# Kernel tuning notes

Hardware: AMD Instinct MI355X
Metric: run time of the kernel (lower is better)

## Reference

```python
import jax, jax.numpy as jnp
import numpy as np
from jax.ops import segment_sum, segment_max

N_NODES = 100000
N_EDGES = 3200000
NODE_FEAT = 128
EDGE_DIM = 8
H = 4          # heads for all three layers
C_HID = 8      # out_layer_1 == out_layer_2 == 8
N_CLASSES = 1
NEG_SLOPE = 0.2


def setup_inputs() -> dict:
    key = jax.random.key(0)
    ks = jax.random.split(key, 20)
    g = lambda k, shape, fan: jax.random.normal(k, shape, jnp.float32) / np.sqrt(fan)
    inp = {
        "x": jax.random.normal(ks[0], (N_NODES, NODE_FEAT), jnp.float32),
        "edge_attr": jax.random.normal(ks[1], (N_EDGES, EDGE_DIM), jnp.float32),
        "edge_index": jax.random.randint(ks[2], (2, N_EDGES), 0, N_NODES, jnp.int32),
        # layer 1: node_feat -> H*C_HID, concat=True, with edge features
        "W1": g(ks[3], (NODE_FEAT, H * C_HID), NODE_FEAT),
        "a_src1": g(ks[4], (H, C_HID), C_HID),
        "a_dst1": g(ks[5], (H, C_HID), C_HID),
        "We1": g(ks[6], (EDGE_DIM, H * C_HID), EDGE_DIM),
        "a_e1": g(ks[7], (H, C_HID), C_HID),
        "b1": jnp.zeros((H * C_HID,), jnp.float32),
        # layer 2: H*C_HID -> C_HID, concat=False
        "W2": g(ks[8], (H * C_HID, H * C_HID), H * C_HID),
        "a_src2": g(ks[9], (H, C_HID), C_HID),
        "a_dst2": g(ks[10], (H, C_HID), C_HID),
        "b2": jnp.zeros((C_HID,), jnp.float32),
        # layer 3: C_HID -> N_CLASSES, concat=False
        "W3": g(ks[11], (C_HID, H * N_CLASSES), C_HID),
        "a_src3": g(ks[12], (H, N_CLASSES), 1),
        "a_dst3": g(ks[13], (H, N_CLASSES), 1),
        "b3": jnp.zeros((N_CLASSES,), jnp.float32),
    }
    return inp


def _gat_conv(x, src, dst, W, a_src, a_dst, bias, concat,
              edge_attr=None, W_edge=None, a_edge=None):
    """PyG GATConv forward (eval mode). src/dst already include self-loops."""
    n = x.shape[0]
    h, c = a_src.shape
    xh = (x @ W).reshape(n, h, c)                       # [N,H,C]
    alpha = (xh * a_src[None]).sum(-1)[src] \
          + (xh * a_dst[None]).sum(-1)[dst]             # [E,H]
    if edge_attr is not None:
        eh = (edge_attr @ W_edge).reshape(-1, h, c)     # [E,H,C]
        alpha = alpha + (eh * a_edge[None]).sum(-1)
    alpha = jax.nn.leaky_relu(alpha, NEG_SLOPE)
    # segment softmax over incoming edges of each dst node
    amax = segment_max(alpha, dst, num_segments=n)       # [N,H]
    ex = jnp.exp(alpha - amax[dst])
    denom = segment_sum(ex, dst, num_segments=n)
    alpha = ex / (denom[dst] + 1e-16)                    # [E,H]
    out = segment_sum(alpha[:, :, None] * xh[src], dst, num_segments=n)  # [N,H,C]
    out = out.reshape(n, h * c) if concat else out.mean(axis=1)
    return out + bias


def _add_self_loops(edge_index, n):
    loop = jnp.arange(n, dtype=edge_index.dtype)
    src = jnp.concatenate([edge_index[0], loop])
    dst = jnp.concatenate([edge_index[1], loop])
    return src, dst


def reference(x, edge_attr, edge_index, W1, a_src1, a_dst1, We1, a_e1, b1,
              W2, a_src2, a_dst2, b2, W3, a_src3, a_dst3, b3):
    n = x.shape[0]
    src, dst = _add_self_loops(edge_index, n)
    # self-loop edge_attr: fill_value='mean' => scatter-mean of edge_attr by dst
    deg = segment_sum(jnp.ones((edge_index.shape[1],), x.dtype), edge_index[1],
                      num_segments=n)
    mean_attr = segment_sum(edge_attr, edge_index[1], num_segments=n) \
              / jnp.maximum(deg, 1.0)[:, None]
    ea = jnp.concatenate([edge_attr, mean_attr], axis=0)

    h = _gat_conv(x, src, dst, W1, a_src1, a_dst1, b1, True,
                  edge_attr=ea, W_edge=We1, a_edge=a_e1)
    h = jax.nn.elu(h)
    h = _gat_conv(h, src, dst, W2, a_src2, a_dst2, b2, False)
    h = jax.nn.elu(h)
    out = _gat_conv(h, src, dst, W3, a_src3, a_dst3, b3, False)
    return out
```

## Files before the change

kernel.cpp:

```cpp
#include <hip/hip_runtime.h>
#include <hip/hip_fp16.h>
#include <cmath>

static inline int cdiv(long a, int b){ return (int)((a + b - 1) / b); }

__device__ __forceinline__ float lrelu(float x){ return x > 0.f ? x : 0.2f * x; }
__device__ __forceinline__ float elu1(float x){ return x > 0.f ? x : expm1f(x); }
__device__ __forceinline__ float fexp(float x){ return __expf(x); }
__device__ __forceinline__ float sel4(float4 v, int h){
  float ab = (h & 1) ? v.y : v.x;
  float cd = (h & 1) ? v.w : v.z;
  return (h & 2) ? cd : ab;
}

#define WAVE_FENCE() do { asm volatile("" ::: "memory"); __builtin_amdgcn_sched_barrier(0); } while(0)

#define W_SHIFT 7
#define BUCKET_N (1 << W_SHIFT)
#define NBMAX   1024
#define NCHUNKS 1024
#define CH_MAX  3136
#define MS_THREADS 1024



__global__ __launch_bounds__(MS_THREADS)
void hist_chunks_kernel(const int* __restrict__ ei, int E, int CH, int* __restrict__ hist2d){
  __shared__ int s_b[NBMAX];
  int t = threadIdx.x, chunk = blockIdx.x;
  s_b[t] = 0;
  __syncthreads();
  int lo = chunk * CH, hi = min(lo + CH, E);
  for (int e = lo + t; e < hi; e += MS_THREADS)
    atomicAdd(&s_b[ei[E + e] >> W_SHIFT], 1);
  __syncthreads();
  hist2d[(size_t)chunk * NBMAX + t] = s_b[t];
}

__global__ __launch_bounds__(NCHUNKS)
void col_scan_kernel(int* __restrict__ hist2d, int* __restrict__ bcnt){
  __shared__ int s[NCHUNKS];
  int b = blockIdx.x, t = threadIdx.x;
  int v = hist2d[(size_t)t * NBMAX + b];
  s[t] = v; __syncthreads();
  #pragma unroll
  for (int off = 1; off < NCHUNKS; off <<= 1){
    int u = (t >= off) ? s[t - off] : 0;
    __syncthreads();
    s[t] += u;
    __syncthreads();
  }
  hist2d[(size_t)t * NBMAX + b] = s[t] - v;
  if (t == NCHUNKS - 1) bcnt[b] = s[t];
}

__global__ void scan_buckets_kernel(const int* __restrict__ bcnt, int nb, int total,
                                    int* __restrict__ bstart, int* __restrict__ row_start, int n){
  __shared__ int s[1024];
  int t = threadIdx.x;
  int v = (t < nb) ? bcnt[t] : 0;
  s[t] = v; __syncthreads();
  #pragma unroll
  for (int off = 1; off < 1024; off <<= 1){
    int u = (t >= off) ? s[t - off] : 0;
    __syncthreads();
    s[t] += u;
    __syncthreads();
  }
  bstart[t] = (t < nb) ? s[t] - v : total;
  if (t == 0){ bstart[NBMAX] = total; row_start[n] = total; }
}

__global__ void wevec_kernel(const float* __restrict__ We, const float* __restrict__ ae,
                             float* __restrict__ wev){
  int i = threadIdx.x;
  if (i >= 32) return;
  int d = i >> 2, h = i & 3;
  float acc = 0.f;
  #pragma unroll
  for (int c = 0; c < 8; ++c) acc = fmaf(We[d * 32 + h * 8 + c], ae[h * 8 + c], acc);
  wev[d * 4 + h] = acc;
}

__global__ __launch_bounds__(MS_THREADS)
void multisplit_kernel(const int* __restrict__ ei, int E, int CH,
                       const float* __restrict__ eattr, const float* __restrict__ wev,
                       const int* __restrict__ bstart, const int* __restrict__ prefix2d,
                       int4* __restrict__ staged){
  __shared__ int4 s_rec[CH_MAX];
  __shared__ int s_fill[NBMAX];
  __shared__ int s_lbase[NBMAX];
  __shared__ int s_shift[NBMAX];
  __shared__ float s_wev[32];
  int t = threadIdx.x, chunk = blockIdx.x;
  if (t < 32) s_wev[t] = wev[t];
  s_fill[t] = 0;
  __syncthreads();
  int lo = chunk * CH, hi = min(lo + CH, E);
  int cnt = hi - lo;
  for (int e = lo + t; e < hi; e += MS_THREADS)
    atomicAdd(&s_fill[ei[E + e] >> W_SHIFT], 1);
  __syncthreads();
  int v = s_fill[t];
  s_lbase[t] = v; __syncthreads();
  #pragma unroll
  for (int off = 1; off < NBMAX; off <<= 1){
    int u = (t >= off) ? s_lbase[t - off] : 0;
    __syncthreads();
    s_lbase[t] += u;
    __syncthreads();
  }
  int excl = s_lbase[t] - v;
  s_lbase[t] = excl;
  s_shift[t] = bstart[t] + prefix2d[(size_t)chunk * NBMAX + t] - excl;
  s_fill[t] = 0;
  __syncthreads();
  for (int e = lo + t; e < hi; e += MS_THREADS){
    int d = ei[E + e];
    int b = d >> W_SHIFT;
    const float4* ea = (const float4*)(eattr + (size_t)e * 8);
    float4 v0 = ea[0], v1 = ea[1];
    float av[8] = {v0.x, v0.y, v0.z, v0.w, v1.x, v1.y, v1.z, v1.w};
    float e0 = 0, e1 = 0, e2 = 0, e3 = 0;
    #pragma unroll
    for (int k = 0; k < 8; ++k){
      e0 = fmaf(av[k], s_wev[k * 4 + 0], e0);
      e1 = fmaf(av[k], s_wev[k * 4 + 1], e1);
      e2 = fmaf(av[k], s_wev[k * 4 + 2], e2);
      e3 = fmaf(av[k], s_wev[k * 4 + 3], e3);
    }
    __half2 h01 = __floats2half2_rn(e0, e1);
    __half2 h23 = __floats2half2_rn(e2, e3);
    int pos = s_lbase[b] + atomicAdd(&s_fill[b], 1);
    s_rec[pos] = make_int4(ei[e], d,
                           __builtin_bit_cast(int, h01), __builtin_bit_cast(int, h23));
  }
  __syncthreads();
  for (int i = t; i < cnt; i += MS_THREADS){
    int4 r = s_rec[i];
    staged[s_shift[r.y >> W_SHIFT] + i] = r;
  }
}

__global__ __launch_bounds__(MS_THREADS)
void bucket_scatter_kernel(const int* __restrict__ bstart, const int4* __restrict__ staged,
                           int n, int* __restrict__ row_start, int* __restrict__ srcs,
                           uint2* __restrict__ escp, float4* __restrict__ selfesc){
  __shared__ int s_cnt[BUCKET_N];
  __shared__ int s_cur[BUCKET_N];
  __shared__ int s_start[BUCKET_N];
  int b = blockIdx.x, t = threadIdx.x;
  int node0 = b << W_SHIFT;
  if (t < BUCKET_N) s_cnt[t] = 0;
  __syncthreads();
  int lo = bstart[b], hi = bstart[b + 1];
  for (int i = lo + t; i < hi; i += MS_THREADS)
    atomicAdd(&s_cnt[staged[i].y & (BUCKET_N - 1)], 1);
  __syncthreads();
  if (t < BUCKET_N) s_cur[t] = s_cnt[t];
  __syncthreads();
  #pragma unroll
  for (int off = 1; off < BUCKET_N; off <<= 1){
    int v = (t < BUCKET_N && t >= off) ? s_cur[t - off] : 0;
    __syncthreads();
    if (t < BUCKET_N) s_cur[t] += v;
    __syncthreads();
  }
  if (t < BUCKET_N){
    int excl = s_cur[t] - s_cnt[t];
    int nd = node0 + t;
    if (nd <= n) row_start[nd] = lo + excl;
    s_start[t] = lo + excl;
    s_cur[t] = lo + excl;
  }
  __syncthreads();
  for (int i = lo + t; i < hi; i += MS_THREADS){
    int4 r = staged[i];
    int pos = atomicAdd(&s_cur[r.y & (BUCKET_N - 1)], 1);
    srcs[pos] = r.x;
    escp[pos] = make_uint2((unsigned)r.z, (unsigned)r.w);
  }
  __syncthreads();
  int nl = t >> 3, sub = t & 7;
  int nd2 = node0 + nl;
  if (nd2 >= n) return;
  int r0 = s_start[nl], r1 = s_start[nl] + s_cnt[nl];
  float e0 = 0, e1 = 0, e2 = 0, e3 = 0;
  for (int k = r0 + sub; k < r1; k += 8){
    uint2 u = escp[k];
    float2 f01 = __half22float2(__builtin_bit_cast(__half2, u.x));
    float2 f23 = __half22float2(__builtin_bit_cast(__half2, u.y));
    e0 += f01.x; e1 += f01.y; e2 += f23.x; e3 += f23.y;
  }
  #pragma unroll
  for (int off = 1; off < 8; off <<= 1){
    e0 += __shfl_xor(e0, off, 64); e1 += __shfl_xor(e1, off, 64);
    e2 += __shfl_xor(e2, off, 64); e3 += __shfl_xor(e3, off, 64);
  }
  if (sub == 0){
    float inv = 1.f / fmaxf((float)s_cnt[nl], 1.f);
    selfesc[nd2] = make_float4(e0 * inv, e1 * inv, e2 * inv, e3 * inv);
  }
}

template<int K>
__global__ __launch_bounds__(256)
void gemm_score_tiled(const float* __restrict__ A, const float* __restrict__ W,
                      const float* __restrict__ asrc, const float* __restrict__ adst,
                      float* __restrict__ out, float* __restrict__ sS,
                      float* __restrict__ sD, int n){
  constexpr int KH = (K > 64) ? 64 : K;
  constexpr int K4 = KH / 4;
  __shared__ float s_AT[KH * 128];
  __shared__ float s_W[K * 32];
  __shared__ float s_as[32], s_ad[32];
  int t = threadIdx.x;
  for (int i = t; i < K * 32; i += 256) s_W[i] = W[i];
  if (t < 32){ s_as[t] = asrc[t]; s_ad[t] = adst[t]; }
  int n0 = blockIdx.x * 128;
  int nrows = min(128, n - n0);
  int rg = t >> 3, q = t & 7;
  float4 acc[4] = {{0,0,0,0},{0,0,0,0},{0,0,0,0},{0,0,0,0}};

  for (int k0 = 0; k0 < K; k0 += KH){
    __syncthreads();
    #pragma unroll
    for (int it = 0; it < 128 * K4 / 256; ++it){
      int idx = t + it * 256;
      int row = idx & 127, k4 = idx >> 7;
      if (row < nrows){
        float4 v = *(const float4*)(A + (size_t)(n0 + row) * K + k0 + 4 * k4);
        s_AT[(4 * k4 + 0) * 128 + row] = v.x;
        s_AT[(4 * k4 + 1) * 128 + row] = v.y;
        s_AT[(4 * k4 + 2) * 128 + row] = v.z;
        s_AT[(4 * k4 + 3) * 128 + row] = v.w;
      }
    }
    __syncthreads();
    #pragma unroll 4
    for (int k = 0; k < KH; ++k){
      float4 a4 = *(const float4*)(s_AT + k * 128 + 4 * rg);
      float4 w4 = *(const float4*)(s_W + (k0 + k) * 32 + 4 * q);
      acc[0].x = fmaf(a4.x, w4.x, acc[0].x); acc[0].y = fmaf(a4.x, w4.y, acc[0].y);
      acc[0].z = fmaf(a4.x, w4.z, acc[0].z); acc[0].w = fmaf(a4.x, w4.w, acc[0].w);
      acc[1].x = fmaf(a4.y, w4.x, acc[1].x); acc[1].y = fmaf(a4.y, w4.y, acc[1].y);
      acc[1].z = fmaf(a4.y, w4.z, acc[1].z); acc[1].w = fmaf(a4.y, w4.w, acc[1].w);
      acc[2].x = fmaf(a4.z, w4.x, acc[2].x); acc[2].y = fmaf(a4.z, w4.y, acc[2].y);
      acc[2].z = fmaf(a4.z, w4.z, acc[2].z); acc[2].w = fmaf(a4.z, w4.w, acc[2].w);
      acc[3].x = fmaf(a4.w, w4.x, acc[3].x); acc[3].y = fmaf(a4.w, w4.y, acc[3].y);
      acc[3].z = fmaf(a4.w, w4.z, acc[3].z); acc[3].w = fmaf(a4.w, w4.w, acc[3].w);
    }
  }

  float as0 = s_as[4 * q + 0], as1 = s_as[4 * q + 1], as2 = s_as[4 * q + 2], as3 = s_as[4 * q + 3];
  float ad0 = s_ad[4 * q + 0], ad1 = s_ad[4 * q + 1], ad2 = s_ad[4 * q + 2], ad3 = s_ad[4 * q + 3];
  #pragma unroll
  for (int i = 0; i < 4; ++i){
    int row = n0 + 4 * rg + i;
    bool ok = (4 * rg + i) < nrows;
    if (ok) ((float4*)out)[(size_t)row * 8 + q] = acc[i];
    float ps = acc[i].x * as0 + acc[i].y * as1 + acc[i].z * as2 + acc[i].w * as3;
    float pd = acc[i].x * ad0 + acc[i].y * ad1 + acc[i].z * ad2 + acc[i].w * ad3;
    ps += __shfl_xor(ps, 1, 64);
    pd += __shfl_xor(pd, 1, 64);
    if (ok && !(q & 1)){
      sS[(size_t)row * 4 + (q >> 1)] = ps;
      sD[(size_t)row * 4 + (q >> 1)] = pd;
    }
  }
}

template<int MODE, bool EDGE>
__global__ void gather_kernel(const int* __restrict__ row_start, const int* __restrict__ srcs,
                              const uint2* __restrict__ escp, const float4* __restrict__ selfesc,
                              const float* __restrict__ sS, const float* __restrict__ sD,
                              const float* __restrict__ xh, const float* __restrict__ bias,
                              float* __restrict__ out, int n,
                              const float* __restrict__ W3p, const float* __restrict__ as3p,
                              const float* __restrict__ ad3p, float* __restrict__ xh3,
                              float* __restrict__ ss3, float* __restrict__ sd3){
  int wv = threadIdx.x >> 6, lane = threadIdx.x & 63;
  int node = blockIdx.x * 4 + wv;

  if constexpr (MODE == 2){
    if (node >= n) return;
    int rs = row_start[node], deg = row_start[node + 1] - rs;
    float4 sd4 = ((const float4*)sD)[node];
    float4 acc = {0,0,0,0}, dsum = {0,0,0,0};
    for (int k = lane; k < deg; k += 64){
      int s = srcs[rs + k];
      float4 ss = ((const float4*)sS)[s];
      float4 w;
      w.x = fexp(lrelu(ss.x + sd4.x)); w.y = fexp(lrelu(ss.y + sd4.y));
      w.z = fexp(lrelu(ss.z + sd4.z)); w.w = fexp(lrelu(ss.w + sd4.w));
      dsum.x += w.x; dsum.y += w.y; dsum.z += w.z; dsum.w += w.w;
      float4 xv = ((const float4*)xh)[s];
      acc.x = fmaf(w.x, xv.x, acc.x); acc.y = fmaf(w.y, xv.y, acc.y);
      acc.z = fmaf(w.z, xv.z, acc.z); acc.w = fmaf(w.w, xv.w, acc.w);
    }
    #pragma unroll
    for (int off = 1; off < 64; off <<= 1){
      acc.x += __shfl_xor(acc.x, off, 64); acc.y += __shfl_xor(acc.y, off, 64);
      acc.z += __shfl_xor(acc.z, off, 64); acc.w += __shfl_xor(acc.w, off, 64);
      dsum.x += __shfl_xor(dsum.x, off, 64); dsum.y += __shfl_xor(dsum.y, off, 64);
      dsum.z += __shfl_xor(dsum.z, off, 64); dsum.w += __shfl_xor(dsum.w, off, 64);
    }
    if (lane == 0){
      float4 ssn = ((const float4*)sS)[node];
      float4 wsf;
      wsf.x = fexp(lrelu(ssn.x + sd4.x)); wsf.y = fexp(lrelu(ssn.y + sd4.y));
      wsf.z = fexp(lrelu(ssn.z + sd4.z)); wsf.w = fexp(lrelu(ssn.w + sd4.w));
      float4 xvn = ((const float4*)xh)[node];
      float v = (acc.x + wsf.x * xvn.x) / (dsum.x + wsf.x + 1e-16f)
              + (acc.y + wsf.y * xvn.y) / (dsum.y + wsf.y + 1e-16f)
              + (acc.z + wsf.z * xvn.z) / (dsum.z + wsf.z + 1e-16f)
              + (acc.w + wsf.w * xvn.w) / (dsum.w + wsf.w + 1e-16f);
      out[node] = 0.25f * v + bias[0];
    }
    return;
  } else {
  __shared__ float4 s_w[4][64];
  __shared__ int    s_src[4][64];
  __shared__ float  s_w3[32];
  __shared__ float  s_a3[8];
  if constexpr (MODE == 1){
    if (threadIdx.x < 32) s_w3[threadIdx.x] = W3p[threadIdx.x];
    if (threadIdx.x < 8)
      s_a3[threadIdx.x] = (threadIdx.x < 4) ? as3p[threadIdx.x] : ad3p[threadIdx.x - 4];
    __syncthreads();
  }
  if (node >= n) return;
  int rs = row_start[node], deg = row_start[node + 1] - rs;
  float4 sd4 = ((const float4*)sD)[node];
  int q = lane & 7;
  int h = q >> 1;
  int sg = lane >> 3;
  float4 acc = {0,0,0,0};
  float dacc = 0.f;

  for (int base = 0; base < deg; base += 64){
    int k = base + lane;
    float4 w = {0,0,0,0}; int s = 0;
    if (k < deg){
      s = srcs[rs + k];
      float4 ss = ((const float4*)sS)[s];
      float a0 = ss.x + sd4.x, a1 = ss.y + sd4.y, a2 = ss.z + sd4.z, a3 = ss.w + sd4.w;
      if constexpr (EDGE){
        uint2 u = escp[rs + k];
        float2 f01 = __half22float2(__builtin_bit_cast(__half2, u.x));
        float2 f23 = __half22float2(__builtin_bit_cast(__half2, u.y));
        a0 += f01.x; a1 += f01.y; a2 += f23.x; a3 += f23.y;
      }
      w.x = fexp(lrelu(a0)); w.y = fexp(lrelu(a1));
      w.z = fexp(lrelu(a2)); w.w = fexp(lrelu(a3));
    }
    s_w[wv][lane] = w;
    s_src[wv][lane] = s;
    WAVE_FENCE();
    int nvalid = min(deg - base, 64);
    const float* s_wf = (const float*)&s_w[wv][0];
    #pragma unroll
    for (int i = 0; i < 8; ++i){
      int slot = i * 8 + sg;
      if (slot < nvalid){
        int s2 = s_src[wv][slot];
        float wg = s_wf[slot * 4 + h];
        float4 xv = ((const float4*)xh)[(size_t)s2 * 8 + q];
        dacc += wg;
        acc.x = fmaf(wg, xv.x, acc.x); acc.y = fmaf(wg, xv.y, acc.y);
        acc.z = fmaf(wg, xv.z, acc.z); acc.w = fmaf(wg, xv.w, acc.w);
      }
    }
    WAVE_FENCE();
  }

  #pragma unroll
  for (int off = 8; off < 64; off <<= 1){
    acc.x += __shfl_xor(acc.x, off, 64); acc.y += __shfl_xor(acc.y, off, 64);
    acc.z += __shfl_xor(acc.z, off, 64); acc.w += __shfl_xor(acc.w, off, 64);
    dacc  += __shfl_xor(dacc,  off, 64);
  }
  float4 ssn = ((const float4*)sS)[node];
  float a_self = sel4(ssn, h) + sel4(sd4, h);
  if constexpr (EDGE) a_self += sel4(selfesc[node], h);
  float wsel = fexp(lrelu(a_self));
  float4 xvn = ((const float4*)xh)[(size_t)node * 8 + q];
  acc.x = fmaf(wsel, xvn.x, acc.x); acc.y = fmaf(wsel, xvn.y, acc.y);
  acc.z = fmaf(wsel, xvn.z, acc.z); acc.w = fmaf(wsel, xvn.w, acc.w);
  dacc += wsel;
  float rin = 1.f / (dacc + 1e-16f);
  float4 val = {acc.x * rin, acc.y * rin, acc.z * rin, acc.w * rin};

  if constexpr (MODE == 0){
    float4 b4 = ((const float4*)bias)[q];
    val.x = elu1(val.x + b4.x); val.y = elu1(val.y + b4.y);
    val.z = elu1(val.z + b4.z); val.w = elu1(val.w + b4.w);
    if (lane < 8) ((float4*)out)[(size_t)node * 8 + lane] = val;
  } else {
    val.x += __shfl_xor(val.x, 2, 64); val.y += __shfl_xor(val.y, 2, 64);
    val.z += __shfl_xor(val.z, 2, 64); val.w += __shfl_xor(val.w, 2, 64);
    val.x += __shfl_xor(val.x, 4, 64); val.y += __shfl_xor(val.y, 4, 64);
    val.z += __shfl_xor(val.z, 4, 64); val.w += __shfl_xor(val.w, 4, 64);
    float4 b4 = ((const float4*)bias)[q & 1];
    val.x = elu1(val.x * 0.25f + b4.x); val.y = elu1(val.y * 0.25f + b4.y);
    val.z = elu1(val.z * 0.25f + b4.z); val.w = elu1(val.w * 0.25f + b4.w);
    float4 oth;
    oth.x = __shfl_xor(val.x, 1, 64); oth.y = __shfl_xor(val.y, 1, 64);
    oth.z = __shfl_xor(val.z, 1, 64); oth.w = __shfl_xor(val.w, 1, 64);
    float h2v[8];
    if (q & 1){
      h2v[0] = oth.x; h2v[1] = oth.y; h2v[2] = oth.z; h2v[3] = oth.w;
      h2v[4] = val.x; h2v[5] = val.y; h2v[6] = val.z; h2v[7] = val.w;
    } else {
      h2v[0] = val.x; h2v[1] = val.y; h2v[2] = val.z; h2v[3] = val.w;
      h2v[4] = oth.x; h2v[5] = oth.y; h2v[6] = oth.z; h2v[7] = oth.w;
    }
    float x3[4];
    #pragma unroll
    for (int j = 0; j < 4; ++j){
      float a = 0.f;
      #pragma unroll
      for (int k = 0; k < 8; ++k) a = fmaf(h2v[k], s_w3[k * 4 + j], a);
      x3[j] = a;
    }
    if (lane == 0){
      ((float4*)xh3)[node] = make_float4(x3[0], x3[1], x3[2], x3[3]);
      ((float4*)ss3)[node] = make_float4(x3[0] * s_a3[0], x3[1] * s_a3[1],
                                         x3[2] * s_a3[2], x3[3] * s_a3[3]);
      ((float4*)sd3)[node] = make_float4(x3[0] * s_a3[4], x3[1] * s_a3[5],
                                         x3[2] * s_a3[6], x3[3] * s_a3[7]);
    }
  }
  }
}


extern "C" void kernel_launch(void* const* d_in, const int* in_sizes, int n_in,
                              void* d_out, int out_size, void* d_ws, size_t ws_size,
                              hipStream_t stream){
  const float* x     = (const float*)d_in[0];
  const float* eattr = (const float*)d_in[1];
  const int*   ei    = (const int*)d_in[2];
  const float* W1  = (const float*)d_in[3];
  const float* as1 = (const float*)d_in[4];
  const float* ad1 = (const float*)d_in[5];
  const float* We1 = (const float*)d_in[6];
  const float* ae1 = (const float*)d_in[7];
  const float* b1  = (const float*)d_in[8];
  const float* W2  = (const float*)d_in[9];
  const float* as2 = (const float*)d_in[10];
  const float* ad2 = (const float*)d_in[11];
  const float* b2  = (const float*)d_in[12];
  const float* W3  = (const float*)d_in[13];
  const float* as3 = (const float*)d_in[14];
  const float* ad3 = (const float*)d_in[15];
  const float* b3  = (const float*)d_in[16];

  const int N = in_sizes[0] / 128;
  const int E = in_sizes[2] / 2;
  const int nb_buckets = (N + BUCKET_N - 1) >> W_SHIFT;
  const int CH = cdiv(E, NCHUNKS);

  char* b0 = (char*)d_ws;
  int4* staged = (int4*)b0;
  float* fp = (float*)b0;
  float* xh = fp; fp += (size_t)N * 32;
  float* sS = fp; fp += (size_t)N * 4;
  float* sD = fp; fp += (size_t)N * 4;
  float* h1 = fp; fp += (size_t)N * 32;
  int*  srcs = (int*)(b0 + (size_t)E * 16);
  uint2* escp = (uint2*)(b0 + (size_t)E * 20);
  int* hist2d = (int*)(b0 + (size_t)E * 28);
  float4* selfesc = (float4*)(hist2d + (size_t)NCHUNKS * NBMAX);
  float* xh3 = (float*)(selfesc + N);
  float* ss3 = xh3 + (size_t)N * 4;
  float* sd3 = ss3 + (size_t)N * 4;
  int* ip = (int*)(sd3 + (size_t)N * 4);
  int* bcnt      = ip; ip += NBMAX;
  int* bstart    = ip; ip += NBMAX + 1;
  int* row_start = ip; ip += N + 1;
  float* wev = (float*)ip;

  const int B = 256;

  wevec_kernel<<<1, 32, 0, stream>>>(We1, ae1, wev);
  hist_chunks_kernel<<<NCHUNKS, MS_THREADS, 0, stream>>>(ei, E, CH, hist2d);
  col_scan_kernel<<<nb_buckets, NCHUNKS, 0, stream>>>(hist2d, bcnt);
  scan_buckets_kernel<<<1, 1024, 0, stream>>>(bcnt, nb_buckets, E, bstart, row_start, N);
  multisplit_kernel<<<NCHUNKS, MS_THREADS, 0, stream>>>(ei, E, CH, eattr, wev, bstart, hist2d, staged);
  bucket_scatter_kernel<<<nb_buckets, MS_THREADS, 0, stream>>>(bstart, staged, N, row_start, srcs, escp, selfesc);

  gemm_score_tiled<128><<<cdiv(N, 128), B, 0, stream>>>(x, W1, as1, ad1, xh, sS, sD, N);
  gather_kernel<0,true><<<cdiv(N, 4), B, 0, stream>>>(row_start, srcs, escp, selfesc, sS, sD, xh, b1, h1, N,
                                                      nullptr, nullptr, nullptr, nullptr, nullptr, nullptr);

  gemm_score_tiled<32><<<cdiv(N, 128), B, 0, stream>>>(h1, W2, as2, ad2, xh, sS, sD, N);
  gather_kernel<1,false><<<cdiv(N, 4), B, 0, stream>>>(row_start, srcs, escp, selfesc, sS, sD, xh, b2, nullptr, N,
                                                       W3, as3, ad3, xh3, ss3, sd3);

  gather_kernel<2,false><<<cdiv(N, 4), B, 0, stream>>>(row_start, srcs, escp, selfesc, ss3, sd3, xh3, b3, (float*)d_out, N,
                                                       nullptr, nullptr, nullptr, nullptr, nullptr, nullptr);
}
```

Baseline: 385.8 us.

## Recompute attention scores in gather from features, drop precomputed score arrays

Removes the precomputed per-node source/destination score arrays. Each gather lane now recomputes the attention logit from the gathered neighbour feature row, using a shuffle to combine half-heads. The attention vectors and edge weights are pre-scaled by log2(e) so exp2 replaces exp, and leaky ReLU becomes a max. The two-phase shared-memory weight staging in the gather is replaced by a direct per-group loop over 8 edges at a time. This cuts one random gather per edge and some GEMM epilogue writes, but adds a few FMAs and a shuffle per edge, plus a cross-lane dependency in the inner loop.

```diff
diff --git a/kernel.cpp b/kernel.cpp
--- a/kernel.cpp
+++ b/kernel.cpp
@@ -4,16 +4,14 @@
 
 static inline int cdiv(long a, int b){ return (int)((a + b - 1) / b); }
 
-__device__ __forceinline__ float lrelu(float x){ return x > 0.f ? x : 0.2f * x; }
+__device__ __forceinline__ float lrelu(float x){ return fmaxf(x, 0.2f * x); }
 __device__ __forceinline__ float elu1(float x){ return x > 0.f ? x : expm1f(x); }
-__device__ __forceinline__ float fexp(float x){ return __expf(x); }
+__device__ __forceinline__ float fexp2(float x){ return exp2f(x); }
 __device__ __forceinline__ float sel4(float4 v, int h){
   float ab = (h & 1) ? v.y : v.x;
   float cd = (h & 1) ? v.w : v.z;
   return (h & 2) ? cd : ab;
 }
-
-#define WAVE_FENCE() do { asm volatile("" ::: "memory"); __builtin_amdgcn_sched_barrier(0); } while(0)
 
 #define W_SHIFT 7
 #define BUCKET_N (1 << W_SHIFT)
@@ -71,15 +69,28 @@
   if (t == 0){ bstart[NBMAX] = total; row_start[n] = total; }
 }
 
-__global__ void wevec_kernel(const float* __restrict__ We, const float* __restrict__ ae,
-                             float* __restrict__ wev){
+__global__ void prep_kernel(const float* __restrict__ We, const float* __restrict__ ae,
+                            const float* __restrict__ as1, const float* __restrict__ ad1,
+                            const float* __restrict__ as2, const float* __restrict__ ad2,
+                            const float* __restrict__ as3, const float* __restrict__ ad3,
+                            float* __restrict__ wev, float* __restrict__ avecs){
+  const float L2E = 1.4426950408889634f;
   int i = threadIdx.x;
-  if (i >= 32) return;
-  int d = i >> 2, h = i & 3;
-  float acc = 0.f;
-  #pragma unroll
-  for (int c = 0; c < 8; ++c) acc = fmaf(We[d * 32 + h * 8 + c], ae[h * 8 + c], acc);
-  wev[d * 4 + h] = acc;
+  if (i < 32){
+    int d = i >> 2, h = i & 3;
+    float acc = 0.f;
+    #pragma unroll
+    for (int c = 0; c < 8; ++c) acc = fmaf(We[d * 32 + h * 8 + c], ae[h * 8 + c], acc);
+    wev[d * 4 + h] = acc * L2E;
+    avecs[i]      = as1[i] * L2E;
+    avecs[32 + i] = ad1[i] * L2E;
+    avecs[64 + i] = as2[i] * L2E;
+    avecs[96 + i] = ad2[i] * L2E;
+  }
+  if (i < 4){
+    avecs[128 + i] = as3[i] * L2E;
+    avecs[132 + i] = ad3[i] * L2E;
+  }
 }
 
 __global__ __launch_bounds__(MS_THREADS)
@@ -205,18 +216,14 @@
 
 template<int K>
 __global__ __launch_bounds__(256)
-void gemm_score_tiled(const float* __restrict__ A, const float* __restrict__ W,
-                      const float* __restrict__ asrc, const float* __restrict__ adst,
-                      float* __restrict__ out, float* __restrict__ sS,
-                      float* __restrict__ sD, int n){
+void gemm_tiled(const float* __restrict__ A, const float* __restrict__ W,
+                float* __restrict__ out, int n){
   constexpr int KH = (K > 64) ? 64 : K;
   constexpr int K4 = KH / 4;
   __shared__ float s_AT[KH * 128];
   __shared__ float s_W[K * 32];
-  __shared__ float s_as[32], s_ad[32];
   int t = threadIdx.x;
   for (int i = t; i < K * 32; i += 256) s_W[i] = W[i];
-  if (t < 32){ s_as[t] = asrc[t]; s_ad[t] = adst[t]; }
   int n0 = blockIdx.x * 128;
   int nrows = min(128, n - n0);
   int rg = t >> 3, q = t & 7;
@@ -251,50 +258,39 @@
       acc[3].z = fmaf(a4.w, w4.z, acc[3].z); acc[3].w = fmaf(a4.w, w4.w, acc[3].w);
     }
   }
-
-  float as0 = s_as[4 * q + 0], as1 = s_as[4 * q + 1], as2 = s_as[4 * q + 2], as3 = s_as[4 * q + 3];
-  float ad0 = s_ad[4 * q + 0], ad1 = s_ad[4 * q + 1], ad2 = s_ad[4 * q + 2], ad3 = s_ad[4 * q + 3];
   #pragma unroll
   for (int i = 0; i < 4; ++i){
     int row = n0 + 4 * rg + i;
-    bool ok = (4 * rg + i) < nrows;
-    if (ok) ((float4*)out)[(size_t)row * 8 + q] = acc[i];
-    float ps = acc[i].x * as0 + acc[i].y * as1 + acc[i].z * as2 + acc[i].w * as3;
-    float pd = acc[i].x * ad0 + acc[i].y * ad1 + acc[i].z * ad2 + acc[i].w * ad3;
-    ps += __shfl_xor(ps, 1, 64);
-    pd += __shfl_xor(pd, 1, 64);
-    if (ok && !(q & 1)){
-      sS[(size_t)row * 4 + (q >> 1)] = ps;
-      sD[(size_t)row * 4 + (q >> 1)] = pd;
-    }
+    if ((4 * rg + i) < nrows) ((float4*)out)[(size_t)row * 8 + q] = acc[i];
   }
 }
 
 template<int MODE, bool EDGE>
 __global__ void gather_kernel(const int* __restrict__ row_start, const int* __restrict__ srcs,
                               const uint2* __restrict__ escp, const float4* __restrict__ selfesc,
-                              const float* __restrict__ sS, const float* __restrict__ sD,
-                              const float* __restrict__ xh, const float* __restrict__ bias,
-                              float* __restrict__ out, int n,
-                              const float* __restrict__ W3p, const float* __restrict__ as3p,
-                              const float* __restrict__ ad3p, float* __restrict__ xh3,
-                              float* __restrict__ ss3, float* __restrict__ sd3){
+                              const float* __restrict__ xh, const float* __restrict__ avq,
+                              const float* __restrict__ bias, float* __restrict__ out, int n,
+                              const float* __restrict__ W3p, float* __restrict__ xh3){
   int wv = threadIdx.x >> 6, lane = threadIdx.x & 63;
   int node = blockIdx.x * 4 + wv;
 
   if constexpr (MODE == 2){
     if (node >= n) return;
     int rs = row_start[node], deg = row_start[node + 1] - rs;
-    float4 sd4 = ((const float4*)sD)[node];
+    float4 a3s = *(const float4*)avq;
+    float4 a3d = *(const float4*)(avq + 4);
+    float4 xvn = ((const float4*)xh)[node];
+    float4 sdn = {xvn.x * a3d.x, xvn.y * a3d.y, xvn.z * a3d.z, xvn.w * a3d.w};
     float4 acc = {0,0,0,0}, dsum = {0,0,0,0};
     for (int k = lane; k < deg; k += 64){
       int s = srcs[rs + k];
-      float4 ss = ((const float4*)sS)[s];
+      float4 xv = ((const float4*)xh)[s];
       float4 w;
-      w.x = fexp(lrelu(ss.x + sd4.x)); w.y = fexp(lrelu(ss.y + sd4.y));
-      w.z = fexp(lrelu(ss.z + sd4.z)); w.w = fexp(lrelu(ss.w + sd4.w));
+      w.x = fexp2(lrelu(fmaf(xv.x, a3s.x, sdn.x)));
+      w.y = fexp2(lrelu(fmaf(xv.y, a3s.y, sdn.y)));
+      w.z = fexp2(lrelu(fmaf(xv.z, a3s.z, sdn.z)));
+      w.w = fexp2(lrelu(fmaf(xv.w, a3s.w, sdn.w)));
       dsum.x += w.x; dsum.y += w.y; dsum.z += w.z; dsum.w += w.w;
-      float4 xv = ((const float4*)xh)[s];
       acc.x = fmaf(w.x, xv.x, acc.x); acc.y = fmaf(w.y, xv.y, acc.y);
       acc.z = fmaf(w.z, xv.z, acc.z); acc.w = fmaf(w.w, xv.w, acc.w);
     }
@@ -306,11 +302,11 @@
       dsum.z += __shfl_xor(dsum.z, off, 64); dsum.w += __shfl_xor(dsum.w, off, 64);
     }
     if (lane == 0){
-      float4 ssn = ((const float4*)sS)[node];
       float4 wsf;
-      wsf.x = fexp(lrelu(ssn.x + sd4.x)); wsf.y = fexp(lrelu(ssn.y + sd4.y));
-      wsf.z = fexp(lrelu(ssn.z + sd4.z)); wsf.w = fexp(lrelu(ssn.w + sd4.w));
-      float4 xvn = ((const float4*)xh)[node];
+      wsf.x = fexp2(lrelu(fmaf(xvn.x, a3s.x, sdn.x)));
+      wsf.y = fexp2(lrelu(fmaf(xvn.y, a3s.y, sdn.y)));
+      wsf.z = fexp2(lrelu(fmaf(xvn.z, a3s.z, sdn.z)));
+      wsf.w = fexp2(lrelu(fmaf(xvn.w, a3s.w, sdn.w)));
       float v = (acc.x + wsf.x * xvn.x) / (dsum.x + wsf.x + 1e-16f)
               + (acc.y + wsf.y * xvn.y) / (dsum.y + wsf.y + 1e-16f)
               + (acc.z + wsf.z * xvn.z) / (dsum.z + wsf.z + 1e-16f)
@@ -319,59 +315,43 @@
     }
     return;
   } else {
-  __shared__ float4 s_w[4][64];
-  __shared__ int    s_src[4][64];
-  __shared__ float  s_w3[32];
-  __shared__ float  s_a3[8];
+  __shared__ float s_w3[32];
   if constexpr (MODE == 1){
     if (threadIdx.x < 32) s_w3[threadIdx.x] = W3p[threadIdx.x];
-    if (threadIdx.x < 8)
-      s_a3[threadIdx.x] = (threadIdx.x < 4) ? as3p[threadIdx.x] : ad3p[threadIdx.x - 4];
     __syncthreads();
   }
   if (node >= n) return;
   int rs = row_start[node], deg = row_start[node + 1] - rs;
-  float4 sd4 = ((const float4*)sD)[node];
-  int q = lane & 7;
-  int h = q >> 1;
-  int sg = lane >> 3;
+  int q = lane & 7, sg = lane >> 3, h = q >> 1;
+  float4 as4 = ((const float4*)avq)[q];
+  float4 ad4 = ((const float4*)(avq + 32))[q];
+  float4 xvn = ((const float4*)xh)[(size_t)node * 8 + q];
+  float pd = xvn.x * ad4.x;
+  pd = fmaf(xvn.y, ad4.y, pd); pd = fmaf(xvn.z, ad4.z, pd); pd = fmaf(xvn.w, ad4.w, pd);
+  float sdh = pd + __shfl_xor(pd, 1, 64);
   float4 acc = {0,0,0,0};
   float dacc = 0.f;
-
-  for (int base = 0; base < deg; base += 64){
-    int k = base + lane;
-    float4 w = {0,0,0,0}; int s = 0;
+  const int* sp = srcs + rs;
+
+  for (int base = 0; base < deg; base += 8){
+    int k = base + sg;
     if (k < deg){
-      s = srcs[rs + k];
-      float4 ss = ((const float4*)sS)[s];
-      float a0 = ss.x + sd4.x, a1 = ss.y + sd4.y, a2 = ss.z + sd4.z, a3 = ss.w + sd4.w;
+      int s = sp[k];
+      float4 xv = ((const float4*)xh)[(size_t)s * 8 + q];
+      float p = xv.x * as4.x;
+      p = fmaf(xv.y, as4.y, p); p = fmaf(xv.z, as4.z, p); p = fmaf(xv.w, as4.w, p);
+      float a = p + __shfl_xor(p, 1, 64) + sdh;
       if constexpr (EDGE){
         uint2 u = escp[rs + k];
         float2 f01 = __half22float2(__builtin_bit_cast(__half2, u.x));
         float2 f23 = __half22float2(__builtin_bit_cast(__half2, u.y));
-        a0 += f01.x; a1 += f01.y; a2 += f23.x; a3 += f23.y;
+        a += (h == 0) ? f01.x : (h == 1) ? f01.y : (h == 2) ? f23.x : f23.y;
       }
-      w.x = fexp(lrelu(a0)); w.y = fexp(lrelu(a1));
-      w.z = fexp(lrelu(a2)); w.w = fexp(lrelu(a3));
-    }
-    s_w[wv][lane] = w;
-    s_src[wv][lane] = s;
-    WAVE_FENCE();
-    int nvalid = min(deg - base, 64);
-    const float* s_wf = (const float*)&s_w[wv][0];
-    #pragma unroll
-    for (int i = 0; i < 8; ++i){
-      int slot = i * 8 + sg;
-      if (slot < nvalid){
-        int s2 = s_src[wv][slot];
-        float wg = s_wf[slot * 4 + h];
-        float4 xv = ((const float4*)xh)[(size_t)s2 * 8 + q];
-        dacc += wg;
-        acc.x = fmaf(wg, xv.x, acc.x); acc.y = fmaf(wg, xv.y, acc.y);
-        acc.z = fmaf(wg, xv.z, acc.z); acc.w = fmaf(wg, xv.w, acc.w);
-      }
-    }
-    WAVE_FENCE();
+      float w = fexp2(lrelu(a));
+      dacc += w;
+      acc.x = fmaf(w, xv.x, acc.x); acc.y = fmaf(w, xv.y, acc.y);
+      acc.z = fmaf(w, xv.z, acc.z); acc.w = fmaf(w, xv.w, acc.w);
+    }
   }
 
   #pragma unroll
@@ -380,11 +360,11 @@
     acc.z += __shfl_xor(acc.z, off, 64); acc.w += __shfl_xor(acc.w, off, 64);
     dacc  += __shfl_xor(dacc,  off, 64);
   }
-  float4 ssn = ((const float4*)sS)[node];
-  float a_self = sel4(ssn, h) + sel4(sd4, h);
+  float p0 = xvn.x * as4.x;
+  p0 = fmaf(xvn.y, as4.y, p0); p0 = fmaf(xvn.z, as4.z, p0); p0 = fmaf(xvn.w, as4.w, p0);
+  float a_self = p0 + __shfl_xor(p0, 1, 64) + sdh;
   if constexpr (EDGE) a_self += sel4(selfesc[node], h);
-  float wsel = fexp(lrelu(a_self));
-  float4 xvn = ((const float4*)xh)[(size_t)node * 8 + q];
+  float wsel = fexp2(lrelu(a_self));
   acc.x = fmaf(wsel, xvn.x, acc.x); acc.y = fmaf(wsel, xvn.y, acc.y);
   acc.z = fmaf(wsel, xvn.z, acc.z); acc.w = fmaf(wsel, xvn.w, acc.w);
   dacc += wsel;
@@ -423,13 +403,8 @@
       for (int k = 0; k < 8; ++k) a = fmaf(h2v[k], s_w3[k * 4 + j], a);
       x3[j] = a;
     }
-    if (lane == 0){
+    if (lane == 0)
       ((float4*)xh3)[node] = make_float4(x3[0], x3[1], x3[2], x3[3]);
-      ((float4*)ss3)[node] = make_float4(x3[0] * s_a3[0], x3[1] * s_a3[1],
-                                         x3[2] * s_a3[2], x3[3] * s_a3[3]);
-      ((float4*)sd3)[node] = make_float4(x3[0] * s_a3[4], x3[1] * s_a3[5],
-                                         x3[2] * s_a3[6], x3[3] * s_a3[7]);
-    }
   }
   }
 }
@@ -465,39 +440,36 @@
   int4* staged = (int4*)b0;
   float* fp = (float*)b0;
   float* xh = fp; fp += (size_t)N * 32;
-  float* sS = fp; fp += (size_t)N * 4;
-  float* sD = fp; fp += (size_t)N * 4;
   float* h1 = fp; fp += (size_t)N * 32;
   int*  srcs = (int*)(b0 + (size_t)E * 16);
   uint2* escp = (uint2*)(b0 + (size_t)E * 20);
   int* hist2d = (int*)(b0 + (size_t)E * 28);
   float4* selfesc = (float4*)(hist2d + (size_t)NCHUNKS * NBMAX);
   float* xh3 = (float*)(selfesc + N);
-  float* ss3 = xh3 + (size_t)N * 4;
-  float* sd3 = ss3 + (size_t)N * 4;
-  int* ip = (int*)(sd3 + (size_t)N * 4);
+  int* ip = (int*)(xh3 + (size_t)N * 4);
   int* bcnt      = ip; ip += NBMAX;
   int* bstart    = ip; ip += NBMAX + 1;
   int* row_start = ip; ip += N + 1;
-  float* wev = (float*)ip;
+  float* wev   = (float*)ip;
+  float* avecs = wev + 32;
 
   const int B = 256;
 
-  wevec_kernel<<<1, 32, 0, stream>>>(We1, ae1, wev);
+  prep_kernel<<<1, 64, 0, stream>>>(We1, ae1, as1, ad1, as2, ad2, as3, ad3, wev, avecs);
   hist_chunks_kernel<<<NCHUNKS, MS_THREADS, 0, stream>>>(ei, E, CH, hist2d);
   col_scan_kernel<<<nb_buckets, NCHUNKS, 0, stream>>>(hist2d, bcnt);
   scan_buckets_kernel<<<1, 1024, 0, stream>>>(bcnt, nb_buckets, E, bstart, row_start, N);
   multisplit_kernel<<<NCHUNKS, MS_THREADS, 0, stream>>>(ei, E, CH, eattr, wev, bstart, hist2d, staged);
   bucket_scatter_kernel<<<nb_buckets, MS_THREADS, 0, stream>>>(bstart, staged, N, row_start, srcs, escp, selfesc);
 
-  gemm_score_tiled<128><<<cdiv(N, 128), B, 0, stream>>>(x, W1, as1, ad1, xh, sS, sD, N);
-  gather_kernel<0,true><<<cdiv(N, 4), B, 0, stream>>>(row_start, srcs, escp, selfesc, sS, sD, xh, b1, h1, N,
-                                                      nullptr, nullptr, nullptr, nullptr, nullptr, nullptr);
-
-  gemm_score_tiled<32><<<cdiv(N, 128), B, 0, stream>>>(h1, W2, as2, ad2, xh, sS, sD, N);
-  gather_kernel<1,false><<<cdiv(N, 4), B, 0, stream>>>(row_start, srcs, escp, selfesc, sS, sD, xh, b2, nullptr, N,
-                                                       W3, as3, ad3, xh3, ss3, sd3);
-
-  gather_kernel<2,false><<<cdiv(N, 4), B, 0, stream>>>(row_start, srcs, escp, selfesc, ss3, sd3, xh3, b3, (float*)d_out, N,
-                                                       nullptr, nullptr, nullptr, nullptr, nullptr, nullptr);
-}
+  gemm_tiled<128><<<cdiv(N, 128), B, 0, stream>>>(x, W1, xh, N);
+  gather_kernel<0,true><<<cdiv(N, 4), B, 0, stream>>>(row_start, srcs, escp, selfesc, xh, avecs,
+                                                      b1, h1, N, nullptr, nullptr);
+
+  gemm_tiled<32><<<cdiv(N, 128), B, 0, stream>>>(h1, W2, xh, N);
+  gather_kernel<1,false><<<cdiv(N, 4), B, 0, stream>>>(row_start, srcs, escp, selfesc, xh, avecs + 64,
+                                                       b2, nullptr, N, W3, xh3);
+
+  gather_kernel<2,false><<<cdiv(N, 4), B, 0, stream>>>(row_start, srcs, escp, selfesc, xh3, avecs + 128,
+                                                       b3, (float*)d_out, N, nullptr, nullptr);
+}
```

Result: no change. 379.1 us (-1.7%).
